# Performance work log

Measured on AMD Instinct MI355X. Metric: run time of the kernel, lower is better.

The kernel has to match this reference:

```python
import jax, jax.numpy as jnp
import numpy as np

B, HP, WP, EMB = 32, 56, 56, 256
HEADS, WX, WY = 8, 7, 7
WS = WX * WY

# relative position index table (constant int lookup, matches torch buffer)
_idx = np.indices((WX, WY)).transpose(1, 2, 0).reshape(WS, 2)
_REL = _idx[None, :, :] - _idx[:, None, :] + np.array([WX - 1, WY - 1])  # [49,49,2]

# shift masks (constants)
_m = WX * (WY // 2)
_row = np.zeros((WS, WS), np.float32)
_row[-_m:, :-_m] = -np.inf
_row[:-_m, -_m:] = -np.inf
# rearrange '(r w1) (c w2) -> (w1 r) (w2 c)' with w1=WX, w2=WY
_col = _row.reshape(WS // WX, WX, WS // WY, WY).transpose(1, 0, 3, 2).reshape(WS, WS)
ROW_MASK = jnp.asarray(_row)
COL_MASK = jnp.asarray(_col)


def setup_inputs() -> dict:
    key = jax.random.key(0)
    k1, k2, k3 = jax.random.split(key, 3)
    x = jax.random.normal(k1, (B, HP, WP, EMB), jnp.float32)
    w1 = jax.random.normal(k2, (EMB, 3 * EMB), jnp.float32) * 0.02
    b1 = jnp.zeros((3 * EMB,), jnp.float32)
    pos_emb = jax.random.normal(k3, (2 * WX - 1, 2 * WY - 1), jnp.float32)
    return {"x": x, "w1": w1, "b1": b1, "pos_emb": pos_emb}


def reference(x, w1, b1, pos_emb):
    Bn, H, W, E = x.shape
    e = E // HEADS
    hdim = float(E) / HEADS
    qkv = x @ w1 + b1                         # [B,H,W,3E]
    qkv = qkv.reshape(Bn, H, W, E, 3)         # (c k): c outer, k inner (interleaved QKV)
    # shifted: roll by (-WX)//2 = -4 for WX=7 (Python floor div, as in source)
    qkv = jnp.roll(qkv, ((-WX) // 2, (-WY) // 2), axis=(1, 2))
    Wh, Ww = H // WX, W // WY
    # split channel (e H): head index is INNER dim, as in source rearrange
    t = qkv.reshape(Bn, Wh, WX, Ww, WY, e, HEADS, 3)
    t = t.transpose(0, 6, 1, 3, 2, 4, 5, 7).reshape(Bn, HEADS, Wh, Ww, WS, e, 3)
    q, k, v = t[..., 0], t[..., 1], t[..., 2]
    attn = jnp.einsum('bhuvqe,bhuvke->bhuvqk', q, k) / jnp.sqrt(
        jnp.asarray(hdim, x.dtype))
    bias = pos_emb[_REL[:, :, 0], _REL[:, :, 1]]   # [49,49]
    attn = attn + bias
    # shift masks on last window row / last window column (corner gets both)
    attn = attn.at[:, :, -1, :, :, :].add(ROW_MASK)
    attn = attn.at[:, :, :, -1, :, :].add(COL_MASK)
    out = jnp.einsum('bhuvqk,bhuvke->bhuvqe', jax.nn.softmax(attn, axis=-1), v)
    # merge back: channel = e*HEADS + h
    out = out.reshape(Bn, HEADS, Wh, Ww, WX, WY, e)
    out = out.transpose(0, 2, 4, 3, 5, 6, 1).reshape(Bn, H, W, E)
    # reverse roll uses WX//2 = +3 (NOT the inverse of -4), faithful to source
    out = jnp.roll(out, (WX // 2, WY // 2), axis=(1, 2))
    return out
```

## Files before the change

kernel.cpp:

```cpp
#include <hip/hip_runtime.h>


typedef short bf16x8 __attribute__((ext_vector_type(8)));
typedef float f32x4 __attribute__((ext_vector_type(4)));
typedef unsigned short u16;
typedef u16 u16x8 __attribute__((ext_vector_type(8)));

#define MFMA16 __builtin_amdgcn_mfma_f32_16x16x32_bf16

__device__ __forceinline__ u16 f2bf(float f) {
  union { float f; unsigned int u; } c; c.f = f;
  unsigned int uu = c.u;
  return (u16)((uu + 0x7fffu + ((uu >> 16) & 1u)) >> 16);
}

#define OFF_A   32768
#define OFF_POS 65536
#define SMEM_BYTES (65536 + 704)

__global__ void prep_w(const float* __restrict__ w1, const float* __restrict__ b1,
                       u16* __restrict__ wT, float* __restrict__ bp) {
  int g = blockIdx.x * 256 + threadIdx.x;
  float val = w1[g];
  int n = g % 768;
  int k = g / 768;
  int t = n % 3, c = n / 3;
  int np = (c & 7) * 96 + t * 32 + (c >> 3);
  wT[np * 256 + k] = f2bf(val);
  if (g < 768) {
    int t2 = g % 3, c2 = g / 3;
    bp[(c2 & 7) * 96 + t2 * 32 + (c2 >> 3)] = b1[g];
  }
}

__launch_bounds__(512, 4)
__global__ void swin_fused(const float* __restrict__ x, const u16* __restrict__ wT,
                           const float* __restrict__ bp, const float* __restrict__ pos,
                           float* __restrict__ out) {
  __shared__ __align__(16) char smem[SMEM_BYTES];
  const int tid  = threadIdx.x;
  const int wave = tid >> 6;
  const int lane = tid & 63;
  const int quad = lane >> 4;
  const int l16  = lane & 15;
  const int blk  = blockIdx.x;
  const int b = blk >> 6, u = (blk >> 3) & 7, v = blk & 7;

  float* sPos = (float*)(smem + OFF_POS);
  if (tid < 169) sPos[tid] = pos[tid];

  {
    const int xbase = b * (56 * 56 * 256);
#pragma unroll
    for (int it = 0; it < 4; ++it) {
      int idx = tid + it * 512;
      int row = idx >> 5;
      int ck  = idx & 31;
      char* dst = smem + OFF_A + row * 512 + ((ck ^ (row & 7)) << 4);
      u16x8 val{};
      if (row < 49) {
        int i = row / 7, j = row % 7;
        int sh = u * 7 + i + 4; if (sh >= 56) sh -= 56;
        int sw = v * 7 + j + 4; if (sw >= 56) sw -= 56;
        const float4* src = (const float4*)(x + xbase + (sh * 56 + sw) * 256 + ck * 8);
        float4 f0 = src[0];
        float4 f1 = src[1];
        val.s0 = f2bf(f0.x); val.s1 = f2bf(f0.y); val.s2 = f2bf(f0.z); val.s3 = f2bf(f0.w);
        val.s4 = f2bf(f1.x); val.s5 = f2bf(f1.y); val.s6 = f2bf(f1.z); val.s7 = f2bf(f1.w);
      }
      *(u16x8*)dst = val;
    }
  }

  float bias[6];
#pragma unroll
  for (int i = 0; i < 6; ++i) bias[i] = bp[wave * 96 + i * 16 + l16];

  __syncthreads();

  const char* sA = smem + OFF_A;
  char* T = smem + wave * 4096;
  bf16x8 qf[4], kf[4], vf[2][2];

#pragma unroll
  for (int t = 0; t < 3; ++t) {
    f32x4 acc[4][2];
#pragma unroll
    for (int m = 0; m < 4; ++m) {
      acc[m][0] = (f32x4){0.f, 0.f, 0.f, 0.f};
      acc[m][1] = (f32x4){0.f, 0.f, 0.f, 0.f};
    }
    const u16* gB0 = wT + (wave * 96 + t * 32 + l16) * 256 + quad * 8;
    const u16* gB1 = gB0 + 16 * 256;
    bf16x8 b0 = *(const bf16x8*)gB0;
    bf16x8 b1 = *(const bf16x8*)gB1;
#pragma unroll
    for (int ks = 0; ks < 8; ++ks) {
      bf16x8 a[4];
#pragma unroll
      for (int m = 0; m < 4; ++m) {
        int row = m * 16 + l16;
        a[m] = *(const bf16x8*)(sA + row * 512 + (((ks * 4 + quad) ^ (row & 7)) << 4));
      }
      bf16x8 b0n, b1n;
      if (ks < 7) {
        b0n = *(const bf16x8*)(gB0 + (ks + 1) * 32);
        b1n = *(const bf16x8*)(gB1 + (ks + 1) * 32);
      }
#pragma unroll
      for (int m = 0; m < 4; ++m) {
        acc[m][0] = MFMA16(a[m], b0, acc[m][0], 0, 0, 0);
        acc[m][1] = MFMA16(a[m], b1, acc[m][1], 0, 0, 0);
      }
      if (ks < 7) { b0 = b0n; b1 = b1n; }
    }

    if (t < 2) {
#pragma unroll
      for (int m = 0; m < 4; ++m)
#pragma unroll
        for (int r = 0; r < 4; ++r) {
          int row = m * 16 + quad * 4 + r;
          int sw = (row >> 2) & 3;
          char* base = T + row * 64;
          *(u16*)(base + ((((l16 >> 3) ^ sw) << 4) | ((l16 & 7) << 1)))
              = f2bf(acc[m][0][r] + bias[t * 2]);
          *(u16*)(base + (((((l16 >> 3) + 2) ^ sw) << 4) | ((l16 & 7) << 1)))
              = f2bf(acc[m][1][r] + bias[t * 2 + 1]);
        }
      asm volatile("s_waitcnt lgkmcnt(0)" ::: "memory");
#pragma unroll
      for (int m = 0; m < 4; ++m) {
        int row = m * 16 + l16;
        const bf16x8 fr = *(const bf16x8*)(T + row * 64 + ((quad ^ ((row >> 2) & 3)) << 4));
        if (t == 0) qf[m] = fr; else kf[m] = fr;
      }
      asm volatile("s_waitcnt lgkmcnt(0)" ::: "memory");
    } else {
#pragma unroll
      for (int m = 0; m < 4; ++m)
#pragma unroll
        for (int r = 0; r < 4; ++r) {
          int key = m * 16 + quad * 4 + r;
          int kc = key >> 3, kb = (key & 7) << 1;
#pragma unroll
          for (int i = 0; i < 2; ++i) {
            int ch = i * 16 + l16;
            *(u16*)(T + ch * 128 + (((kc ^ (ch & 7)) << 4) | kb))
                = f2bf(acc[m][i][r] + bias[4 + i]);
          }
        }
      asm volatile("s_waitcnt lgkmcnt(0)" ::: "memory");
    }
  }

  float rsum[4][4];
  f32x4 o[4][2];
  {
    f32x4 s[4][4];
#pragma unroll
    for (int m = 0; m < 4; ++m)
#pragma unroll
      for (int n = 0; n < 4; ++n) s[m][n] = (f32x4){0.f, 0.f, 0.f, 0.f};
#pragma unroll
    for (int m = 0; m < 4; ++m)
#pragma unroll
      for (int n = 0; n < 4; ++n)
        s[m][n] = MFMA16(qf[m], kf[n], s[m][n], 0, 0, 0);

#pragma unroll
    for (int ph = 0; ph < 2; ++ph)
#pragma unroll
      for (int n = 0; n < 2; ++n) {
        int ch = n * 16 + l16;
        vf[ph][n] = *(const bf16x8*)(T + ch * 128 + (((ph * 4 + quad) ^ (ch & 7)) << 4));
      }
    asm volatile("s_waitcnt lgkmcnt(0)" ::: "memory");

    const bool rowm = (u == 7), colm = (v == 7);
    int ki[4], kj[4]; bool kok[4], kro[4], kco[4];
#pragma unroll
    for (int n = 0; n < 4; ++n) {
      int k = n * 16 + l16;
      ki[n] = k / 7; kj[n] = k % 7;
      kok[n] = (k < 49);
      kro[n] = (ki[n] >= 4);
      kco[n] = (kj[n] >= 4);
    }
    const float scale = 0.17677669529663687f;
#pragma unroll
    for (int m = 0; m < 4; ++m) {
#pragma unroll
      for (int r = 0; r < 4; ++r) {
        int q = m * 16 + quad * 4 + r;
        int qi = q / 7, qj = q % 7;
        bool qro = (qi >= 4), qco = (qj >= 4);
        float vmax = -3e30f;
#pragma unroll
        for (int n = 0; n < 4; ++n) {
          bool bad = (!kok[n]) || (rowm && (qro != kro[n])) || (colm && (qco != kco[n]));
          float sv = bad ? -1e30f
                         : s[m][n][r] * scale + sPos[(ki[n] - qi + 6) * 13 + (kj[n] - qj + 6)];
          s[m][n][r] = sv;
          vmax = fmaxf(vmax, sv);
        }
        vmax = fmaxf(vmax, __shfl_xor(vmax, 1));
        vmax = fmaxf(vmax, __shfl_xor(vmax, 2));
        vmax = fmaxf(vmax, __shfl_xor(vmax, 4));
        vmax = fmaxf(vmax, __shfl_xor(vmax, 8));
        float sum = 0.f;
#pragma unroll
        for (int n = 0; n < 4; ++n) {
          float p = __expf(s[m][n][r] - vmax);
          s[m][n][r] = p;
          sum += p;
        }
        sum += __shfl_xor(sum, 1);
        sum += __shfl_xor(sum, 2);
        sum += __shfl_xor(sum, 4);
        sum += __shfl_xor(sum, 8);
        rsum[m][r] = sum;
      }
    }

#pragma unroll
    for (int m = 0; m < 4; ++m) { o[m][0] = (f32x4){0.f,0.f,0.f,0.f}; o[m][1] = (f32x4){0.f,0.f,0.f,0.f}; }

#pragma unroll
    for (int ph = 0; ph < 2; ++ph) {
#pragma unroll
      for (int n2 = 0; n2 < 2; ++n2) {
        int n  = ph * 2 + n2;
        int kh = n2 * 16 + l16;
        int kb = (kh & 7) << 1;
#pragma unroll
        for (int m = 0; m < 4; ++m)
#pragma unroll
          for (int r = 0; r < 4; ++r) {
            int row = m * 16 + quad * 4 + r;
            *(u16*)(T + row * 64 + ((((kh >> 3) ^ ((row >> 2) & 3)) << 4) | kb)) = f2bf(s[m][n][r]);
          }
      }
      asm volatile("s_waitcnt lgkmcnt(0)" ::: "memory");
      bf16x8 pa[4];
#pragma unroll
      for (int m = 0; m < 4; ++m) {
        int row = m * 16 + l16;
        pa[m] = *(const bf16x8*)(T + row * 64 + ((quad ^ ((row >> 2) & 3)) << 4));
      }
#pragma unroll
      for (int m = 0; m < 4; ++m)
#pragma unroll
        for (int n = 0; n < 2; ++n)
          o[m][n] = MFMA16(pa[m], vf[ph][n], o[m][n], 0, 0, 0);
    }
  }

  __syncthreads();
  {
    float* oLds = (float*)smem;
    const int hh = wave;
#pragma unroll
    for (int m = 0; m < 4; ++m)
#pragma unroll
      for (int r = 0; r < 4; ++r) {
        int row = m * 16 + quad * 4 + r;
        if (row < 49) {
          float inv = 1.f / rsum[m][r];
#pragma unroll
          for (int n = 0; n < 2; ++n) {
            int ci = n * 32 + l16 * 2 + (hh >> 2);
            int cs = ci ^ ((ci >> 3) & 3);
            oLds[row * 260 + cs * 4 + (hh & 3)] = o[m][n][r] * inv;
          }
        }
      }
  }
  __syncthreads();
  {
    const int obase = b * (56 * 56 * 256);
    for (int i = tid; i < 49 * 64; i += 512) {
      int row = i >> 6, ck = i & 63;
      int ii = row / 7, jj = row % 7;
      int dh = u * 7 + ii + 3; if (dh >= 56) dh -= 56;
      int dw = v * 7 + jj + 3; if (dw >= 56) dw -= 56;
      f32x4 val = *(const f32x4*)((const float*)smem + row * 260 + 4 * (ck ^ ((ck >> 3) & 3)));
      *(f32x4*)(out + obase + (dh * 56 + dw) * 256 + ck * 4) = val;
    }
  }
}

extern "C" void kernel_launch(void* const* d_in, const int* in_sizes, int n_in,
                              void* d_out, int out_size, void* d_ws, size_t ws_size,
                              hipStream_t stream) {
  const float* x   = (const float*)d_in[0];
  const float* w1  = (const float*)d_in[1];
  const float* b1  = (const float*)d_in[2];
  const float* pos = (const float*)d_in[3];
  const size_t need = (size_t)768 * 256 * 2 + 768 * 4;
  if (ws_size < need) return;
  u16*   wT = (u16*)d_ws;
  float* bp = (float*)((char*)d_ws + 768 * 256 * 2);
  prep_w<<<768, 256, 0, stream>>>(w1, b1, wT, bp);
  swin_fused<<<2048, 512, 0, stream>>>(x, wT, bp, pos, (float*)d_out);
}
```

Before: 342.7 us.

## Replace LDS round-trips with register shuffles and transposed MFMA operands in fused Swin attention

```diff
diff --git a/kernel.cpp b/kernel.cpp
--- a/kernel.cpp
+++ b/kernel.cpp
@@ -6,7 +6,7 @@
 typedef unsigned short u16;
 typedef u16 u16x8 __attribute__((ext_vector_type(8)));
 
-#define MFMA16 __builtin_amdgcn_mfma_f32_16x16x32_bf16
+#define MFMA16(A, B, C) __builtin_amdgcn_mfma_f32_16x16x32_bf16((A), (B), (C), 0, 0, 0)
 
 __device__ __forceinline__ u16 f2bf(float f) {
   union { float f; unsigned int u; } c; c.f = f;
@@ -14,9 +14,30 @@
   return (u16)((uu + 0x7fffu + ((uu >> 16) & 1u)) >> 16);
 }
 
-#define OFF_A   32768
-#define OFF_POS 65536
-#define SMEM_BYTES (65536 + 704)
+__device__ __forceinline__ unsigned int cvtpk(float lo, float hi) {
+  unsigned int r;
+  asm("v_cvt_pk_bf16_f32 %0, %1, %2" : "=v"(r) : "v"(lo), "v"(hi));
+  return r;
+}
+
+__device__ __forceinline__ bf16x8 xchg(unsigned int p0a, unsigned int p1a,
+                                       unsigned int p0b, unsigned int p1b,
+                                       int quad, int l16) {
+  int lo = ((quad & 1) << 5) | l16;
+  int hi = lo + 16;
+  int a0 = __shfl((int)p0a, lo), b0 = __shfl((int)p0b, lo);
+  int a1 = __shfl((int)p1a, lo), b1 = __shfl((int)p1b, lo);
+  int a2 = __shfl((int)p0a, hi), b2 = __shfl((int)p0b, hi);
+  int a3 = __shfl((int)p1a, hi), b3 = __shfl((int)p1b, hi);
+  bool h = quad >= 2;
+  union { int u[4]; bf16x8 v; } r;
+  r.u[0] = h ? b0 : a0; r.u[1] = h ? b1 : a1;
+  r.u[2] = h ? b2 : a2; r.u[3] = h ? b3 : a3;
+  return r.v;
+}
+
+#define OFF_POS 50960
+#define SMEM_BYTES (50960 + 688)
 
 __global__ void prep_w(const float* __restrict__ w1, const float* __restrict__ b1,
                        u16* __restrict__ wT, float* __restrict__ bp) {
@@ -56,7 +77,7 @@
       int idx = tid + it * 512;
       int row = idx >> 5;
       int ck  = idx & 31;
-      char* dst = smem + OFF_A + row * 512 + ((ck ^ (row & 7)) << 4);
+      char* dst = smem + row * 512 + ((ck ^ (row & 7)) << 4);
       u16x8 val{};
       if (row < 49) {
         int i = row / 7, j = row % 7;
@@ -72,14 +93,17 @@
     }
   }
 
-  float bias[6];
-#pragma unroll
-  for (int i = 0; i < 6; ++i) bias[i] = bp[wave * 96 + i * 16 + l16];
+  f32x4 bqk[2][2];
+#pragma unroll
+  for (int t = 0; t < 2; ++t)
+#pragma unroll
+    for (int i = 0; i < 2; ++i)
+      bqk[t][i] = *(const f32x4*)(bp + wave * 96 + t * 32 + i * 16 + quad * 4);
+  float bv[2] = { bp[wave * 96 + 64 + l16], bp[wave * 96 + 80 + l16] };
 
   __syncthreads();
 
-  const char* sA = smem + OFF_A;
-  char* T = smem + wave * 4096;
+  const char* sA = smem;
   bf16x8 qf[4], kf[4], vf[2][2];
 
 #pragma unroll
@@ -107,184 +131,155 @@
         b0n = *(const bf16x8*)(gB0 + (ks + 1) * 32);
         b1n = *(const bf16x8*)(gB1 + (ks + 1) * 32);
       }
+      if (t < 2) {
+#pragma unroll
+        for (int m = 0; m < 4; ++m) {
+          acc[m][0] = MFMA16(b0, a[m], acc[m][0]);
+          acc[m][1] = MFMA16(b1, a[m], acc[m][1]);
+        }
+      } else {
+#pragma unroll
+        for (int m = 0; m < 4; ++m) {
+          acc[m][0] = MFMA16(a[m], b0, acc[m][0]);
+          acc[m][1] = MFMA16(a[m], b1, acc[m][1]);
+        }
+      }
+      if (ks < 7) { b0 = b0n; b1 = b1n; }
+    }
+
+    if (t < 2) {
 #pragma unroll
       for (int m = 0; m < 4; ++m) {
-        acc[m][0] = MFMA16(a[m], b0, acc[m][0], 0, 0, 0);
-        acc[m][1] = MFMA16(a[m], b1, acc[m][1], 0, 0, 0);
-      }
-      if (ks < 7) { b0 = b0n; b1 = b1n; }
-    }
-
-    if (t < 2) {
+        unsigned int p0i0 = cvtpk(acc[m][0][0] + bqk[t][0][0], acc[m][0][1] + bqk[t][0][1]);
+        unsigned int p1i0 = cvtpk(acc[m][0][2] + bqk[t][0][2], acc[m][0][3] + bqk[t][0][3]);
+        unsigned int p0i1 = cvtpk(acc[m][1][0] + bqk[t][1][0], acc[m][1][1] + bqk[t][1][1]);
+        unsigned int p1i1 = cvtpk(acc[m][1][2] + bqk[t][1][2], acc[m][1][3] + bqk[t][1][3]);
+        bf16x8 fr = xchg(p0i0, p1i0, p0i1, p1i1, quad, l16);
+        if (t == 0) qf[m] = fr; else kf[m] = fr;
+      }
+    } else {
+      unsigned int pv0[4][2], pv1[4][2];
 #pragma unroll
       for (int m = 0; m < 4; ++m)
 #pragma unroll
+        for (int i = 0; i < 2; ++i) {
+          pv0[m][i] = cvtpk(acc[m][i][0] + bv[i], acc[m][i][1] + bv[i]);
+          pv1[m][i] = cvtpk(acc[m][i][2] + bv[i], acc[m][i][3] + bv[i]);
+        }
+#pragma unroll
+      for (int ph = 0; ph < 2; ++ph)
+#pragma unroll
+        for (int i = 0; i < 2; ++i)
+          vf[ph][i] = xchg(pv0[2 * ph][i], pv1[2 * ph][i],
+                           pv0[2 * ph + 1][i], pv1[2 * ph + 1][i], quad, l16);
+    }
+  }
+
+  unsigned int pb[4], fl[4];
+#pragma unroll
+  for (int n = 0; n < 4; ++n) {
+    pb[n] = 0; fl[n] = 0;
+#pragma unroll
+    for (int r = 0; r < 4; ++r) {
+      int k = n * 16 + quad * 4 + r;
+      int ki = k / 7, kj = k % 7;
+      bool kok = (k < 49);
+      pb[n] |= (unsigned int)(kok ? ki * 13 + kj : 0) << (8 * r);
+      fl[n] |= ((unsigned int)kok << r) | ((unsigned int)(ki >= 4) << (8 + r))
+             | ((unsigned int)(kj >= 4) << (16 + r));
+    }
+  }
+  const bool rowm = (u == 7), colm = (v == 7);
+  const float scale = 0.17677669529663687f;
+
+  __syncthreads();
+
+  float* oLds = (float*)smem;
+#pragma unroll
+  for (int m = 0; m < 4; ++m) {
+    f32x4 st[4];
+#pragma unroll
+    for (int n = 0; n < 4; ++n)
+      st[n] = MFMA16(kf[n], qf[m], ((f32x4){0.f, 0.f, 0.f, 0.f}));
+
+    const int q = m * 16 + l16;
+    const int qi = q / 7, qj = q % 7;
+    const int cm = 84 - qi * 13 - qj;
+    const bool qro = (qi >= 4), qco = (qj >= 4);
+
+    float mx = -3e30f;
+#pragma unroll
+    for (int n = 0; n < 4; ++n)
+#pragma unroll
+      for (int r = 0; r < 4; ++r) {
+        bool kok = (fl[n] >> r) & 1;
+        bool kro = (fl[n] >> (8 + r)) & 1;
+        bool kco = (fl[n] >> (16 + r)) & 1;
+        bool bad = (!kok) || (rowm && (qro != kro)) || (colm && (qco != kco));
+        int pidx = (int)((pb[n] >> (8 * r)) & 255) + cm;
+        float sv = bad ? -1e30f : st[n][r] * scale + sPos[pidx];
+        st[n][r] = sv;
+        mx = fmaxf(mx, sv);
+      }
+    mx = fmaxf(mx, __shfl_xor(mx, 16));
+    mx = fmaxf(mx, __shfl_xor(mx, 32));
+    float sum = 0.f;
+#pragma unroll
+    for (int n = 0; n < 4; ++n)
+#pragma unroll
+      for (int r = 0; r < 4; ++r) {
+        float p = __expf(st[n][r] - mx);
+        st[n][r] = p;
+        sum += p;
+      }
+    sum += __shfl_xor(sum, 16);
+    sum += __shfl_xor(sum, 32);
+
+    unsigned int pk0[4], pk1[4];
+#pragma unroll
+    for (int n = 0; n < 4; ++n) {
+      pk0[n] = cvtpk(st[n][0], st[n][1]);
+      pk1[n] = cvtpk(st[n][2], st[n][3]);
+    }
+    bf16x8 pa0 = xchg(pk0[0], pk1[0], pk0[1], pk1[1], quad, l16);
+    bf16x8 pa1 = xchg(pk0[2], pk1[2], pk0[3], pk1[3], quad, l16);
+
+    f32x4 ot[2];
+#pragma unroll
+    for (int i = 0; i < 2; ++i) {
+      ot[i] = MFMA16(vf[0][i], pa0, ((f32x4){0.f, 0.f, 0.f, 0.f}));
+      ot[i] = MFMA16(vf[1][i], pa1, ot[i]);
+    }
+
+    if (q < 49) {
+      float inv = 1.f / sum;
+#pragma unroll
+      for (int i = 0; i < 2; ++i)
+#pragma unroll
         for (int r = 0; r < 4; ++r) {
-          int row = m * 16 + quad * 4 + r;
-          int sw = (row >> 2) & 3;
-          char* base = T + row * 64;
-          *(u16*)(base + ((((l16 >> 3) ^ sw) << 4) | ((l16 & 7) << 1)))
-              = f2bf(acc[m][0][r] + bias[t * 2]);
-          *(u16*)(base + (((((l16 >> 3) + 2) ^ sw) << 4) | ((l16 & 7) << 1)))
-              = f2bf(acc[m][1][r] + bias[t * 2 + 1]);
+          int ch  = i * 16 + quad * 4 + r;
+          int col = ch * 8 + wave;
+          int c2  = col ^ ((col >> 5) & 3);
+          oLds[q * 260 + c2] = ot[i][r] * inv;
         }
-      asm volatile("s_waitcnt lgkmcnt(0)" ::: "memory");
-#pragma unroll
-      for (int m = 0; m < 4; ++m) {
-        int row = m * 16 + l16;
-        const bf16x8 fr = *(const bf16x8*)(T + row * 64 + ((quad ^ ((row >> 2) & 3)) << 4));
-        if (t == 0) qf[m] = fr; else kf[m] = fr;
-      }
-      asm volatile("s_waitcnt lgkmcnt(0)" ::: "memory");
-    } else {
-#pragma unroll
-      for (int m = 0; m < 4; ++m)
-#pragma unroll
-        for (int r = 0; r < 4; ++r) {
-          int key = m * 16 + quad * 4 + r;
-          int kc = key >> 3, kb = (key & 7) << 1;
-#pragma unroll
-          for (int i = 0; i < 2; ++i) {
-            int ch = i * 16 + l16;
-            *(u16*)(T + ch * 128 + (((kc ^ (ch & 7)) << 4) | kb))
-                = f2bf(acc[m][i][r] + bias[4 + i]);
-          }
-        }
-      asm volatile("s_waitcnt lgkmcnt(0)" ::: "memory");
-    }
-  }
-
-  float rsum[4][4];
-  f32x4 o[4][2];
-  {
-    f32x4 s[4][4];
-#pragma unroll
-    for (int m = 0; m < 4; ++m)
-#pragma unroll
-      for (int n = 0; n < 4; ++n) s[m][n] = (f32x4){0.f, 0.f, 0.f, 0.f};
-#pragma unroll
-    for (int m = 0; m < 4; ++m)
-#pragma unroll
-      for (int n = 0; n < 4; ++n)
-        s[m][n] = MFMA16(qf[m], kf[n], s[m][n], 0, 0, 0);
-
-#pragma unroll
-    for (int ph = 0; ph < 2; ++ph)
-#pragma unroll
-      for (int n = 0; n < 2; ++n) {
-        int ch = n * 16 + l16;
-        vf[ph][n] = *(const bf16x8*)(T + ch * 128 + (((ph * 4 + quad) ^ (ch & 7)) << 4));
-      }
-    asm volatile("s_waitcnt lgkmcnt(0)" ::: "memory");
-
-    const bool rowm = (u == 7), colm = (v == 7);
-    int ki[4], kj[4]; bool kok[4], kro[4], kco[4];
-#pragma unroll
-    for (int n = 0; n < 4; ++n) {
-      int k = n * 16 + l16;
-      ki[n] = k / 7; kj[n] = k % 7;
-      kok[n] = (k < 49);
-      kro[n] = (ki[n] >= 4);
-      kco[n] = (kj[n] >= 4);
-    }
-    const float scale = 0.17677669529663687f;
-#pragma unroll
-    for (int m = 0; m < 4; ++m) {
-#pragma unroll
-      for (int r = 0; r < 4; ++r) {
-        int q = m * 16 + quad * 4 + r;
-        int qi = q / 7, qj = q % 7;
-        bool qro = (qi >= 4), qco = (qj >= 4);
-        float vmax = -3e30f;
-#pragma unroll
-        for (int n = 0; n < 4; ++n) {
-          bool bad = (!kok[n]) || (rowm && (qro != kro[n])) || (colm && (qco != kco[n]));
-          float sv = bad ? -1e30f
-                         : s[m][n][r] * scale + sPos[(ki[n] - qi + 6) * 13 + (kj[n] - qj + 6)];
-          s[m][n][r] = sv;
-          vmax = fmaxf(vmax, sv);
-        }
-        vmax = fmaxf(vmax, __shfl_xor(vmax, 1));
-        vmax = fmaxf(vmax, __shfl_xor(vmax, 2));
-        vmax = fmaxf(vmax, __shfl_xor(vmax, 4));
-        vmax = fmaxf(vmax, __shfl_xor(vmax, 8));
-        float sum = 0.f;
-#pragma unroll
-        for (int n = 0; n < 4; ++n) {
-          float p = __expf(s[m][n][r] - vmax);
-          s[m][n][r] = p;
-          sum += p;
-        }
-        sum += __shfl_xor(sum, 1);
-        sum += __shfl_xor(sum, 2);
-        sum += __shfl_xor(sum, 4);
-        sum += __shfl_xor(sum, 8);
-        rsum[m][r] = sum;
-      }
-    }
-
-#pragma unroll
-    for (int m = 0; m < 4; ++m) { o[m][0] = (f32x4){0.f,0.f,0.f,0.f}; o[m][1] = (f32x4){0.f,0.f,0.f,0.f}; }
-
-#pragma unroll
-    for (int ph = 0; ph < 2; ++ph) {
-#pragma unroll
-      for (int n2 = 0; n2 < 2; ++n2) {
-        int n  = ph * 2 + n2;
-        int kh = n2 * 16 + l16;
-        int kb = (kh & 7) << 1;
-#pragma unroll
-        for (int m = 0; m < 4; ++m)
-#pragma unroll
-          for (int r = 0; r < 4; ++r) {
-            int row = m * 16 + quad * 4 + r;
-            *(u16*)(T + row * 64 + ((((kh >> 3) ^ ((row >> 2) & 3)) << 4) | kb)) = f2bf(s[m][n][r]);
-          }
-      }
-      asm volatile("s_waitcnt lgkmcnt(0)" ::: "memory");
-      bf16x8 pa[4];
-#pragma unroll
-      for (int m = 0; m < 4; ++m) {
-        int row = m * 16 + l16;
-        pa[m] = *(const bf16x8*)(T + row * 64 + ((quad ^ ((row >> 2) & 3)) << 4));
-      }
-#pragma unroll
-      for (int m = 0; m < 4; ++m)
-#pragma unroll
-        for (int n = 0; n < 2; ++n)
-          o[m][n] = MFMA16(pa[m], vf[ph][n], o[m][n], 0, 0, 0);
-    }
-  }
-
+    }
+  }
   __syncthreads();
-  {
-    float* oLds = (float*)smem;
-    const int hh = wave;
-#pragma unroll
-    for (int m = 0; m < 4; ++m)
-#pragma unroll
-      for (int r = 0; r < 4; ++r) {
-        int row = m * 16 + quad * 4 + r;
-        if (row < 49) {
-          float inv = 1.f / rsum[m][r];
-#pragma unroll
-          for (int n = 0; n < 2; ++n) {
-            int ci = n * 32 + l16 * 2 + (hh >> 2);
-            int cs = ci ^ ((ci >> 3) & 3);
-            oLds[row * 260 + cs * 4 + (hh & 3)] = o[m][n][r] * inv;
-          }
-        }
-      }
-  }
-  __syncthreads();
+
   {
     const int obase = b * (56 * 56 * 256);
-    for (int i = tid; i < 49 * 64; i += 512) {
-      int row = i >> 6, ck = i & 63;
+    for (int i2 = tid; i2 < 49 * 64; i2 += 512) {
+      int row = i2 >> 6, ck = i2 & 63;
       int ii = row / 7, jj = row % 7;
       int dh = u * 7 + ii + 3; if (dh >= 56) dh -= 56;
       int dw = v * 7 + jj + 3; if (dw >= 56) dw -= 56;
-      f32x4 val = *(const f32x4*)((const float*)smem + row * 260 + 4 * (ck ^ ((ck >> 3) & 3)));
+      f32x4 val;
+#pragma unroll
+      for (int e = 0; e < 4; ++e) {
+        int col = ck * 4 + e;
+        int c2  = col ^ ((col >> 5) & 3);
+        val[e] = oLds[row * 260 + c2];
+      }
       *(f32x4*)(out + obase + (dh * 56 + dw) * 256 + ck * 4) = val;
     }
   }
```

Result: slower. 510.2 us (+48.9%).
